# Optimization experiments

Measured on AMD Instinct MI355X. Metric: run time of the kernel, lower is better.

## Reference

```python
import jax, jax.numpy as jnp
import numpy as np

B, S, D, H, PAST = 8, 1, 1024, 16, 8192
HD = D // H


def _rotate_half(x):
    x1, x2 = jnp.split(x, 2, axis=-1)
    return jnp.concatenate([-x2, x1], axis=-1)


def setup_inputs() -> dict:
    key = jax.random.key(0)
    ks = jax.random.split(key, 8)
    s = 0.02  # realistic weight init scale
    return {
        "x": jax.random.normal(ks[0], (B, S, D), jnp.float32),
        "Wq": jax.random.normal(ks[1], (D, D), jnp.float32) * s,
        "bq": jnp.zeros((D,), jnp.float32),
        "Wk": jax.random.normal(ks[2], (D, D), jnp.float32) * s,
        "bk": jnp.zeros((D,), jnp.float32),
        "Wv": jax.random.normal(ks[3], (D, D), jnp.float32) * s,
        "bv": jnp.zeros((D,), jnp.float32),
        "Wo": jax.random.normal(ks[4], (D, D), jnp.float32) * s,
        "bo": jnp.zeros((D,), jnp.float32),
        "past_k": jax.random.normal(ks[5], (B, H, PAST, HD), jnp.float32),
        "past_v": jax.random.normal(ks[6], (B, H, PAST, HD), jnp.float32),
    }


def reference(x, Wq, bq, Wk, bk, Wv, bv, Wo, bo, past_k, past_v):
    b, s, d = x.shape
    h = H
    hd = d // h

    def proj(W, bias):
        # (b, s, d) -> (b, h, s, hd)
        return (x @ W.T + bias).reshape(b, s, h, hd).transpose(0, 2, 1, 3)

    q = proj(Wq, bq)
    k = proj(Wk, bk)
    v = proj(Wv, bv)

    # RoPE with positions offset by cache length (rotate-half convention, base 10000)
    past_len = past_k.shape[2]
    pos = (past_len + jnp.arange(s)).astype(jnp.float32)  # (s,)
    inv_freq = 1.0 / (10000.0 ** (jnp.arange(0, hd, 2, dtype=jnp.float32) / hd))  # (hd/2,)
    ang = pos[:, None] * inv_freq[None, :]  # (s, hd/2)
    cos = jnp.concatenate([jnp.cos(ang), jnp.cos(ang)], axis=-1)[None, None]  # (1,1,s,hd)
    sin = jnp.concatenate([jnp.sin(ang), jnp.sin(ang)], axis=-1)[None, None]
    q = q * cos + _rotate_half(q) * sin
    k = k * cos + _rotate_half(k) * sin

    # KV-cache append (cache holds post-RoPE keys)
    k = jnp.concatenate([past_k, k], axis=2)  # (b, h, past+s, hd)
    v = jnp.concatenate([past_v, v], axis=2)

    # SDPA; S == 1 so is_causal is False per `use_causal_mask and S > 1`
    scale = 1.0 / jnp.sqrt(jnp.asarray(hd, jnp.float32))
    scores = jnp.einsum('bhqd,bhkd->bhqk', q, k) * scale
    attn = jax.nn.softmax(scores, axis=-1)
    out = jnp.einsum('bhqk,bhkd->bhqd', attn, v)  # (b, h, s, hd)
    out = out.transpose(0, 2, 1, 3).reshape(b, s, d)
    return out @ Wo.T + bo
```

## Files before the change

### kernel.cpp

```cpp
#include <hip/hip_runtime.h>
#include <hip/hip_bf16.h>
#include <math.h>

#define BB 8
#define HH 16
#define DD 1024
#define HD 64
#define PAST 8192
#define PAIRS (BB*HH)
#define CHUNKS 8
#define CHUNK (PAST/CHUNKS)
#define PART_STRIDE 66

__global__ __launch_bounds__(256) void qkv_kernel(
    const float* __restrict__ x,
    const float* __restrict__ Wq, const float* __restrict__ bq,
    const float* __restrict__ Wk, const float* __restrict__ bk,
    const float* __restrict__ Wv, const float* __restrict__ bv,
    float* __restrict__ qkv)
{
    int wid  = blockIdx.x * 4 + (threadIdx.x >> 6);
    int lane = threadIdx.x & 63;
    int mat  = wid >> 13;
    int rem  = wid & 8191;
    int b    = rem >> 10;
    int j    = rem & 1023;
    const float* W    = (mat == 0) ? Wq : ((mat == 1) ? Wk : Wv);
    const float* bias = (mat == 0) ? bq : ((mat == 1) ? bk : bv);
    const float* xr = x + b * DD;
    const float* wr = W + (size_t)j * DD;
    float sum = 0.f;
    #pragma unroll
    for (int t = 0; t < 4; ++t) {
        float4 w4 = *(const float4*)(wr + t * 256 + lane * 4);
        float4 x4 = *(const float4*)(xr + t * 256 + lane * 4);
        sum = fmaf(x4.x, w4.x, sum);
        sum = fmaf(x4.y, w4.y, sum);
        sum = fmaf(x4.z, w4.z, sum);
        sum = fmaf(x4.w, w4.w, sum);
    }
    #pragma unroll
    for (int m = 32; m; m >>= 1) sum += __shfl_xor(sum, m);
    if (lane == 0)
        qkv[mat * (BB * DD) + b * DD + j] = sum + bias[j];
}

__global__ __launch_bounds__(256) void rope_kernel(float* __restrict__ qkv)
{
    int tid = blockIdx.x * blockDim.x + threadIdx.x;
    if (tid >= PAIRS * (HD / 2)) return;
    int i  = tid & 31;
    int bh = tid >> 5;
    float invf = (float)pow(10000.0, -(double)i / 32.0);
    float angf = (float)PAST * invf;
    double ang = (double)angf;
    float c = (float)cos(ang), s = (float)sin(ang);
    float* q = qkv + bh * HD;
    float* k = qkv + BB * DD + bh * HD;
    float q0 = q[i], q1 = q[i + 32];
    q[i]      = q0 * c - q1 * s;
    q[i + 32] = q1 * c + q0 * s;
    float k0 = k[i], k1 = k[i + 32];
    k[i]      = k0 * c - k1 * s;
    k[i + 32] = k1 * c + k0 * s;
}

__global__ __launch_bounds__(256) void attn_part_kernel(
    const float* __restrict__ past_k, const float* __restrict__ past_v,
    const float* __restrict__ qkv, float* __restrict__ part)
{
    int pair  = blockIdx.x >> 3;
    int chunk = blockIdx.x & 7;
    int wave  = threadIdx.x >> 6;
    int lane  = threadIdx.x & 63;
    int g     = lane >> 3;
    int sl    = (lane & 7) * 8;

    const float* q = qkv + pair * HD;
    float ql[8];
    #pragma unroll
    for (int t = 0; t < 8; ++t) ql[t] = q[sl + t] * 0.125f;

    const float* kbase = past_k + ((size_t)pair * PAST + (size_t)chunk * CHUNK) * HD;
    const float* vbase = past_v + ((size_t)pair * PAST + (size_t)chunk * CHUNK) * HD;

    float m_run = -1e30f, l_run = 0.f;
    float acc[8];
    #pragma unroll
    for (int t = 0; t < 8; ++t) acc[t] = 0.f;

    for (int i = 0; i < CHUNK / 32; ++i) {
        int key = i * 32 + wave * 8 + g;
        const float* kp = kbase + (size_t)key * HD + sl;
        const float* vp = vbase + (size_t)key * HD + sl;
        float4 k0 = *(const float4*)(kp);
        float4 k1 = *(const float4*)(kp + 4);
        float4 v0 = *(const float4*)(vp);
        float4 v1 = *(const float4*)(vp + 4);
        float s = 0.f;
        s = fmaf(ql[0], k0.x, s); s = fmaf(ql[1], k0.y, s);
        s = fmaf(ql[2], k0.z, s); s = fmaf(ql[3], k0.w, s);
        s = fmaf(ql[4], k1.x, s); s = fmaf(ql[5], k1.y, s);
        s = fmaf(ql[6], k1.z, s); s = fmaf(ql[7], k1.w, s);
        s += __shfl_xor(s, 1); s += __shfl_xor(s, 2); s += __shfl_xor(s, 4);
        float mt = s;
        mt = fmaxf(mt, __shfl_xor(mt, 8));
        mt = fmaxf(mt, __shfl_xor(mt, 16));
        mt = fmaxf(mt, __shfl_xor(mt, 32));
        float m_new = fmaxf(m_run, mt);
        float corr  = __expf(m_run - m_new);
        float p     = __expf(s - m_new);
        float psum  = p;
        psum += __shfl_xor(psum, 8); psum += __shfl_xor(psum, 16); psum += __shfl_xor(psum, 32);
        l_run = l_run * corr + psum;
        m_run = m_new;
        acc[0] = fmaf(acc[0], corr, p * v0.x);
        acc[1] = fmaf(acc[1], corr, p * v0.y);
        acc[2] = fmaf(acc[2], corr, p * v0.z);
        acc[3] = fmaf(acc[3], corr, p * v0.w);
        acc[4] = fmaf(acc[4], corr, p * v1.x);
        acc[5] = fmaf(acc[5], corr, p * v1.y);
        acc[6] = fmaf(acc[6], corr, p * v1.z);
        acc[7] = fmaf(acc[7], corr, p * v1.w);
    }
    #pragma unroll
    for (int t = 0; t < 8; ++t) {
        acc[t] += __shfl_xor(acc[t], 8);
        acc[t] += __shfl_xor(acc[t], 16);
        acc[t] += __shfl_xor(acc[t], 32);
    }
    __shared__ float s_o[4][64];
    __shared__ float s_m[4], s_l[4];
    if (lane < 8) {
        #pragma unroll
        for (int t = 0; t < 8; ++t) s_o[wave][lane * 8 + t] = acc[t];
    }
    if (lane == 0) { s_m[wave] = m_run; s_l[wave] = l_run; }
    __syncthreads();
    if (threadIdx.x < 64) {
        int d = threadIdx.x;
        float m = fmaxf(fmaxf(s_m[0], s_m[1]), fmaxf(s_m[2], s_m[3]));
        float l = 0.f, o = 0.f;
        #pragma unroll
        for (int w = 0; w < 4; ++w) {
            float e = __expf(s_m[w] - m);
            l += s_l[w] * e;
            o += s_o[w][d] * e;
        }
        float* pp = part + (size_t)blockIdx.x * PART_STRIDE;
        pp[2 + d] = o;
        if (d == 0) { pp[0] = m; pp[1] = l; }
    }
}

__global__ __launch_bounds__(64) void attn_reduce_kernel(
    const float* __restrict__ part, const float* __restrict__ qkv,
    float* __restrict__ attn)
{
    int pair = blockIdx.x;
    int d    = threadIdx.x;
    const float* q  = qkv + pair * HD;
    const float* kn = qkv + BB * DD + pair * HD;
    const float* vn = qkv + 2 * BB * DD + pair * HD;
    float s = q[d] * kn[d];
    #pragma unroll
    for (int m = 32; m; m >>= 1) s += __shfl_xor(s, m);
    s *= 0.125f;
    const float* pp = part + (size_t)pair * CHUNKS * PART_STRIDE;
    float m = s;
    for (int c = 0; c < CHUNKS; ++c) m = fmaxf(m, pp[c * PART_STRIDE]);
    float en = __expf(s - m);
    float l = en;
    float o = en * vn[d];
    for (int c = 0; c < CHUNKS; ++c) {
        float e = __expf(pp[c * PART_STRIDE] - m);
        l += pp[c * PART_STRIDE + 1] * e;
        o += pp[c * PART_STRIDE + 2 + d] * e;
    }
    attn[pair * HD + d] = o / l;
}

__global__ __launch_bounds__(256) void oproj_kernel(
    const float* __restrict__ attn, const float* __restrict__ Wo,
    const float* __restrict__ bo, float* __restrict__ out)
{
    int wid  = blockIdx.x * 4 + (threadIdx.x >> 6);
    int lane = threadIdx.x & 63;
    int b = wid >> 10, j = wid & 1023;
    const float* ar = attn + b * DD;
    const float* wr = Wo + (size_t)j * DD;
    float sum = 0.f;
    #pragma unroll
    for (int t = 0; t < 4; ++t) {
        float4 w4 = *(const float4*)(wr + t * 256 + lane * 4);
        float4 a4 = *(const float4*)(ar + t * 256 + lane * 4);
        sum = fmaf(a4.x, w4.x, sum);
        sum = fmaf(a4.y, w4.y, sum);
        sum = fmaf(a4.z, w4.z, sum);
        sum = fmaf(a4.w, w4.w, sum);
    }
    #pragma unroll
    for (int m = 32; m; m >>= 1) sum += __shfl_xor(sum, m);
    if (lane == 0)
        out[b * DD + j] = sum + bo[j];
}

extern "C" void kernel_launch(void* const* d_in, const int* in_sizes, int n_in,
                              void* d_out, int out_size, void* d_ws, size_t ws_size,
                              hipStream_t stream) {
    const float* x      = (const float*)d_in[0];
    const float* Wq     = (const float*)d_in[1];
    const float* bq     = (const float*)d_in[2];
    const float* Wk     = (const float*)d_in[3];
    const float* bk     = (const float*)d_in[4];
    const float* Wv     = (const float*)d_in[5];
    const float* bv     = (const float*)d_in[6];
    const float* Wo     = (const float*)d_in[7];
    const float* bo     = (const float*)d_in[8];
    const float* past_k = (const float*)d_in[9];
    const float* past_v = (const float*)d_in[10];
    float* out = (float*)d_out;

    float* qkv  = (float*)d_ws;
    float* part = qkv + 3 * BB * DD;
    float* attn = part + PAIRS * CHUNKS * PART_STRIDE;

    qkv_kernel<<<3 * BB * DD / 4, 256, 0, stream>>>(x, Wq, bq, Wk, bk, Wv, bv, qkv);
    rope_kernel<<<16, 256, 0, stream>>>(qkv);
    attn_part_kernel<<<PAIRS * CHUNKS, 256, 0, stream>>>(past_k, past_v, qkv, part);
    attn_reduce_kernel<<<PAIRS, 64, 0, stream>>>(part, qkv, attn);
    oproj_kernel<<<BB * DD / 4, 256, 0, stream>>>(attn, Wo, bo, out);
}
```

Baseline: 544.9 us.

## Split attention into two-pass scores/softmax then PV with more chunks

Doubles the number of KV chunks per (batch, head) pair to 16, giving 2048 blocks instead of 1024. Inside each block the online-softmax loop is replaced by two passes. The first computes all scores into shared memory and takes a block max; the second exponentiates once and accumulates P·V without per-step rescaling. This removes the per-key max/sum shuffles and correction exponentials from the hot loop and adds parallelism. In exchange it adds two block barriers and writes twice as many partial results for the reduce kernel.

```diff
diff --git a/kernel.cpp b/kernel.cpp
--- a/kernel.cpp
+++ b/kernel.cpp
@@ -8,7 +8,7 @@
 #define HD 64
 #define PAST 8192
 #define PAIRS (BB*HH)
-#define CHUNKS 8
+#define CHUNKS 16
 #define CHUNK (PAST/CHUNKS)
 #define PART_STRIDE 66
 
@@ -69,13 +69,18 @@
     const float* __restrict__ past_k, const float* __restrict__ past_v,
     const float* __restrict__ qkv, float* __restrict__ part)
 {
-    int pair  = blockIdx.x >> 3;
-    int chunk = blockIdx.x & 7;
+    int pair  = blockIdx.x >> 4;
+    int chunk = blockIdx.x & 15;
     int wave  = threadIdx.x >> 6;
     int lane  = threadIdx.x & 63;
     int g     = lane >> 3;
     int sl    = (lane & 7) * 8;
 
+    __shared__ float s_p[CHUNK];
+    __shared__ float s_m[4];
+    __shared__ float red_o[4][64];
+    __shared__ float red_l[4];
+
     const float* q = qkv + pair * HD;
     float ql[8];
     #pragma unroll
@@ -84,44 +89,60 @@
     const float* kbase = past_k + ((size_t)pair * PAST + (size_t)chunk * CHUNK) * HD;
     const float* vbase = past_v + ((size_t)pair * PAST + (size_t)chunk * CHUNK) * HD;
 
-    float m_run = -1e30f, l_run = 0.f;
-    float acc[8];
-    #pragma unroll
-    for (int t = 0; t < 8; ++t) acc[t] = 0.f;
-
+    float m_loc = -1e30f;
+    #pragma unroll 2
     for (int i = 0; i < CHUNK / 32; ++i) {
         int key = i * 32 + wave * 8 + g;
         const float* kp = kbase + (size_t)key * HD + sl;
-        const float* vp = vbase + (size_t)key * HD + sl;
         float4 k0 = *(const float4*)(kp);
         float4 k1 = *(const float4*)(kp + 4);
-        float4 v0 = *(const float4*)(vp);
-        float4 v1 = *(const float4*)(vp + 4);
         float s = 0.f;
         s = fmaf(ql[0], k0.x, s); s = fmaf(ql[1], k0.y, s);
         s = fmaf(ql[2], k0.z, s); s = fmaf(ql[3], k0.w, s);
         s = fmaf(ql[4], k1.x, s); s = fmaf(ql[5], k1.y, s);
         s = fmaf(ql[6], k1.z, s); s = fmaf(ql[7], k1.w, s);
         s += __shfl_xor(s, 1); s += __shfl_xor(s, 2); s += __shfl_xor(s, 4);
-        float mt = s;
-        mt = fmaxf(mt, __shfl_xor(mt, 8));
-        mt = fmaxf(mt, __shfl_xor(mt, 16));
-        mt = fmaxf(mt, __shfl_xor(mt, 32));
-        float m_new = fmaxf(m_run, mt);
-        float corr  = __expf(m_run - m_new);
-        float p     = __expf(s - m_new);
-        float psum  = p;
-        psum += __shfl_xor(psum, 8); psum += __shfl_xor(psum, 16); psum += __shfl_xor(psum, 32);
-        l_run = l_run * corr + psum;
-        m_run = m_new;
-        acc[0] = fmaf(acc[0], corr, p * v0.x);
-        acc[1] = fmaf(acc[1], corr, p * v0.y);
-        acc[2] = fmaf(acc[2], corr, p * v0.z);
-        acc[3] = fmaf(acc[3], corr, p * v0.w);
-        acc[4] = fmaf(acc[4], corr, p * v1.x);
-        acc[5] = fmaf(acc[5], corr, p * v1.y);
-        acc[6] = fmaf(acc[6], corr, p * v1.z);
-        acc[7] = fmaf(acc[7], corr, p * v1.w);
+        m_loc = fmaxf(m_loc, s);
+        if ((lane & 7) == 0) s_p[key] = s;
+    }
+    m_loc = fmaxf(m_loc, __shfl_xor(m_loc, 8));
+    m_loc = fmaxf(m_loc, __shfl_xor(m_loc, 16));
+    m_loc = fmaxf(m_loc, __shfl_xor(m_loc, 32));
+    if (lane == 0) s_m[wave] = m_loc;
+    __syncthreads();
+    float mblk = fmaxf(fmaxf(s_m[0], s_m[1]), fmaxf(s_m[2], s_m[3]));
+
+    {
+        int t0 = threadIdx.x;
+        float p0 = __expf(s_p[t0] - mblk);
+        float p1 = __expf(s_p[t0 + 256] - mblk);
+        s_p[t0]       = p0;
+        s_p[t0 + 256] = p1;
+        float l_part = p0 + p1;
+        #pragma unroll
+        for (int m = 32; m; m >>= 1) l_part += __shfl_xor(l_part, m);
+        if (lane == 0) red_l[wave] = l_part;
+    }
+    __syncthreads();
+
+    float acc[8];
+    #pragma unroll
+    for (int t = 0; t < 8; ++t) acc[t] = 0.f;
+    #pragma unroll 4
+    for (int i = 0; i < CHUNK / 32; ++i) {
+        int key = i * 32 + wave * 8 + g;
+        const float* vp = vbase + (size_t)key * HD + sl;
+        float4 v0 = *(const float4*)(vp);
+        float4 v1 = *(const float4*)(vp + 4);
+        float p = s_p[key];
+        acc[0] = fmaf(p, v0.x, acc[0]);
+        acc[1] = fmaf(p, v0.y, acc[1]);
+        acc[2] = fmaf(p, v0.z, acc[2]);
+        acc[3] = fmaf(p, v0.w, acc[3]);
+        acc[4] = fmaf(p, v1.x, acc[4]);
+        acc[5] = fmaf(p, v1.y, acc[5]);
+        acc[6] = fmaf(p, v1.z, acc[6]);
+        acc[7] = fmaf(p, v1.w, acc[7]);
     }
     #pragma unroll
     for (int t = 0; t < 8; ++t) {
@@ -129,27 +150,20 @@
         acc[t] += __shfl_xor(acc[t], 16);
         acc[t] += __shfl_xor(acc[t], 32);
     }
-    __shared__ float s_o[4][64];
-    __shared__ float s_m[4], s_l[4];
     if (lane < 8) {
         #pragma unroll
-        for (int t = 0; t < 8; ++t) s_o[wave][lane * 8 + t] = acc[t];
-    }
-    if (lane == 0) { s_m[wave] = m_run; s_l[wave] = l_run; }
+        for (int t = 0; t < 8; ++t) red_o[wave][lane * 8 + t] = acc[t];
+    }
     __syncthreads();
     if (threadIdx.x < 64) {
         int d = threadIdx.x;
-        float m = fmaxf(fmaxf(s_m[0], s_m[1]), fmaxf(s_m[2], s_m[3]));
-        float l = 0.f, o = 0.f;
-        #pragma unroll
-        for (int w = 0; w < 4; ++w) {
-            float e = __expf(s_m[w] - m);
-            l += s_l[w] * e;
-            o += s_o[w][d] * e;
-        }
+        float o = red_o[0][d] + red_o[1][d] + red_o[2][d] + red_o[3][d];
         float* pp = part + (size_t)blockIdx.x * PART_STRIDE;
         pp[2 + d] = o;
-        if (d == 0) { pp[0] = m; pp[1] = l; }
+        if (d == 0) {
+            pp[0] = mblk;
+            pp[1] = red_l[0] + red_l[1] + red_l[2] + red_l[3];
+        }
     }
 }
 
```

Measured after the change: 551.3 us. No clear change (+1.2%).
